# Performance work log

Measured on AMD Instinct MI355X. Metric: run time of the kernel, lower is better.

## Reference

```python
import jax, jax.numpy as jnp
import numpy as np

B, L, D, H = 2, 2048, 512, 8
SAMPLING_FACTOR = 5


def setup_inputs() -> dict:
    key = jax.random.key(0)
    ks = jax.random.split(key, 12)
    L_K = min(8000, L)
    log_L_K = int(np.ceil(np.log1p(L_K)))
    U_part = min(SAMPLING_FACTOR * L * log_L_K, L_K)  # = 2048
    inp = {
        'q': jax.random.normal(ks[0], (B, L, D), jnp.float32),
        'k': jax.random.normal(ks[1], (B, L, D), jnp.float32),
        'v': jax.random.normal(ks[2], (B, L, D), jnp.float32),
        'Wq': jax.random.normal(ks[3], (D, D), jnp.float32) * 0.02,
        'bq': jnp.zeros((D,), jnp.float32),
        'Wk': jax.random.normal(ks[4], (D, D), jnp.float32) * 0.02,
        'bk': jnp.zeros((D,), jnp.float32),
        'Wv': jax.random.normal(ks[5], (D, D), jnp.float32) * 0.02,
        'bv': jnp.zeros((D,), jnp.float32),
        'Wo': jax.random.normal(ks[6], (D, D), jnp.float32) * 0.02,
        'bo': jnp.zeros((D,), jnp.float32),
        'index_sample': jax.random.randint(ks[7], (U_part,), 0, L_K, jnp.int32),
    }
    return inp


def _prob_sparse(qh, Kh, Vh, index_sample):
    # qh, Kh, Vh: [B, H, L, d]
    L_K = min(8000, Kh.shape[2])  # K_sample = K[:, :8000]; L_K = its length
    L_Q = qh.shape[2]
    Ks = Kh[:, :, index_sample, :]                                  # [B,H,U,d]
    QKs = jnp.einsum('bhqd,bhkd->bhqk', qh, Ks)                     # [B,H,Lq,U]
    # M = max - sum/L_K  (source divides by L_K, not U_part)
    M = QKs.max(axis=-1) - QKs.sum(axis=-1) / L_K                   # [B,H,Lq]
    u = min(SAMPLING_FACTOR * int(np.ceil(np.log1p(L_Q))), L_Q)     # = 40
    _, M_top = jax.lax.top_k(-M, u)                                 # topk(largest=False)
    Q_red = jnp.take_along_axis(qh, M_top[..., None], axis=2)       # [B,H,u,d]
    d_k = qh.shape[-1]
    scores = jnp.einsum('bhqd,bhkd->bhqk', Q_red, Kh) / jnp.sqrt(jnp.asarray(d_k, qh.dtype))
    probs = jax.nn.softmax(scores, axis=-1)
    out = jnp.einsum('bhqk,bhkd->bhqd', probs, Vh)                  # [B,H,u,d]
    return out, scores


def reference(q, k, v, Wq, bq, Wk, bk, Wv, bv, Wo, bo, index_sample):
    qp = q @ Wq.T + bq
    kp = k @ Wk.T + bk
    vp = v @ Wv.T + bv
    Bsz, Lq, Dm = qp.shape
    d = Dm // H
    # faithful to source: q is view'd to [B,H,Lq,d] WITHOUT transpose
    qh = qp.reshape(Bsz, H, Lq, d)
    kh = kp.reshape(Bsz, -1, H, d).transpose(0, 2, 1, 3)
    vh = vp.reshape(Bsz, -1, H, d).transpose(0, 2, 1, 3)
    out, _ = _prob_sparse(qh, kh, vh, index_sample)
    u = out.shape[2]
    out = out.transpose(0, 2, 1, 3).reshape(Bsz, u, Dm)             # concat
    return out @ Wo.T + bo                                          # [B,u,D]
```

## Files before the change

### kernel.cpp

```cpp
#include <hip/hip_runtime.h>
#include <math.h>

#define B_ 2
#define L_ 2048
#define D_ 512
#define H_ 8
#define DH 64
#define NS 2048
#define NU 40
#define BHD (L_*D_)
#define QHS (L_*DH)

typedef __attribute__((ext_vector_type(8))) short bf16x8;
typedef __attribute__((ext_vector_type(4))) float f32x4;

__device__ inline float4 ld4(const float* p) { return *reinterpret_cast<const float4*>(p); }

__device__ inline unsigned short hi16(float x) { return (unsigned short)(__float_as_uint(x) >> 16); }
__device__ inline float trunchf(float x) { return __uint_as_float(__float_as_uint(x) & 0xFFFF0000u); }
__device__ inline void tsplit(float x, unsigned short& hs, unsigned short& ms, unsigned short& ls) {
  float h = trunchf(x); hs = hi16(x);
  float r = x - h;
  float m = trunchf(r); ms = hi16(r);
  float r2 = r - m;
  ls = hi16(r2);
}

__global__ __launch_bounds__(256) void proj_mfma(
    const float* __restrict__ qa, const float* __restrict__ ka, const float* __restrict__ va,
    const float* __restrict__ Wq, const float* __restrict__ Wk, const float* __restrict__ Wv,
    const float* __restrict__ bq, const float* __restrict__ bk, const float* __restrict__ bv,
    float* __restrict__ qp, float* __restrict__ kp, float* __restrict__ vp)
{
  __shared__ __align__(16) unsigned short a3[3][128][36];
  __shared__ __align__(16) unsigned short w3[3][128][36];
  const int t = threadIdx.x;
  const int mat = blockIdx.z;
  const float* A    = (mat == 0) ? qa : (mat == 1) ? ka : va;
  const float* W    = (mat == 0) ? Wq : (mat == 1) ? Wk : Wv;
  const float* bias = (mat == 0) ? bq : (mat == 1) ? bk : bv;
  float* C          = (mat == 0) ? qp : (mat == 1) ? kp : vp;
  const int m0 = blockIdx.x * 128, n0 = blockIdx.y * 128;
  const int w = t >> 6, l = t & 63;
  const int wm = w >> 1, wn = w & 1;
  const int lr = l & 15, lg = l >> 4;
  const int srow = t >> 1, sc0 = (t & 1) * 16;

  f32x4 acc[4][4];
#pragma unroll
  for (int i = 0; i < 4; ++i)
#pragma unroll
    for (int j = 0; j < 4; ++j) acc[i][j] = (f32x4){0.f, 0.f, 0.f, 0.f};

  for (int kc = 0; kc < 16; ++kc) {
    const int kb = kc * 32;
    __syncthreads();
    {
      const float* src = A + (size_t)(m0 + srow) * 512 + kb + sc0;
      float xs[16];
#pragma unroll
      for (int i = 0; i < 4; ++i) {
        float4 v4 = ld4(src + 4*i);
        xs[4*i] = v4.x; xs[4*i+1] = v4.y; xs[4*i+2] = v4.z; xs[4*i+3] = v4.w;
      }
#pragma unroll
      for (int hh = 0; hh < 2; ++hh) {
        union { bf16x8 v; unsigned short u[8]; } H, M, L;
#pragma unroll
        for (int e = 0; e < 8; ++e) tsplit(xs[hh*8 + e], H.u[e], M.u[e], L.u[e]);
        *reinterpret_cast<bf16x8*>(&a3[0][srow][sc0 + 8*hh]) = H.v;
        *reinterpret_cast<bf16x8*>(&a3[1][srow][sc0 + 8*hh]) = M.v;
        *reinterpret_cast<bf16x8*>(&a3[2][srow][sc0 + 8*hh]) = L.v;
      }
    }
    {
      const float* src = W + (size_t)(n0 + srow) * 512 + kb + sc0;
      float xs[16];
#pragma unroll
      for (int i = 0; i < 4; ++i) {
        float4 v4 = ld4(src + 4*i);
        xs[4*i] = v4.x; xs[4*i+1] = v4.y; xs[4*i+2] = v4.z; xs[4*i+3] = v4.w;
      }
#pragma unroll
      for (int hh = 0; hh < 2; ++hh) {
        union { bf16x8 v; unsigned short u[8]; } H, M, L;
#pragma unroll
        for (int e = 0; e < 8; ++e) tsplit(xs[hh*8 + e], H.u[e], M.u[e], L.u[e]);
        *reinterpret_cast<bf16x8*>(&w3[0][srow][sc0 + 8*hh]) = H.v;
        *reinterpret_cast<bf16x8*>(&w3[1][srow][sc0 + 8*hh]) = M.v;
        *reinterpret_cast<bf16x8*>(&w3[2][srow][sc0 + 8*hh]) = L.v;
      }
    }
    __syncthreads();

    bf16x8 af[3][4], bf[3][4];
#pragma unroll
    for (int p = 0; p < 3; ++p)
#pragma unroll
      for (int mi = 0; mi < 4; ++mi)
        af[p][mi] = *reinterpret_cast<const bf16x8*>(&a3[p][wm*64 + mi*16 + lr][lg*8]);
#pragma unroll
    for (int p = 0; p < 3; ++p)
#pragma unroll
      for (int ni = 0; ni < 4; ++ni)
        bf[p][ni] = *reinterpret_cast<const bf16x8*>(&w3[p][wn*64 + ni*16 + lr][lg*8]);
#pragma unroll
    for (int mi = 0; mi < 4; ++mi)
#pragma unroll
      for (int ni = 0; ni < 4; ++ni) {
        acc[mi][ni] = __builtin_amdgcn_mfma_f32_16x16x32_bf16(af[0][mi], bf[0][ni], acc[mi][ni], 0, 0, 0);
        acc[mi][ni] = __builtin_amdgcn_mfma_f32_16x16x32_bf16(af[0][mi], bf[1][ni], acc[mi][ni], 0, 0, 0);
        acc[mi][ni] = __builtin_amdgcn_mfma_f32_16x16x32_bf16(af[1][mi], bf[0][ni], acc[mi][ni], 0, 0, 0);
        acc[mi][ni] = __builtin_amdgcn_mfma_f32_16x16x32_bf16(af[1][mi], bf[1][ni], acc[mi][ni], 0, 0, 0);
        acc[mi][ni] = __builtin_amdgcn_mfma_f32_16x16x32_bf16(af[0][mi], bf[2][ni], acc[mi][ni], 0, 0, 0);
        acc[mi][ni] = __builtin_amdgcn_mfma_f32_16x16x32_bf16(af[2][mi], bf[0][ni], acc[mi][ni], 0, 0, 0);
      }
  }
#pragma unroll
  for (int mi = 0; mi < 4; ++mi)
#pragma unroll
    for (int ni = 0; ni < 4; ++ni) {
      const int gn = n0 + wn*64 + ni*16 + lr;
      const float bv_ = bias[gn];
#pragma unroll
      for (int r = 0; r < 4; ++r) {
        const int gm = m0 + wm*64 + mi*16 + lg*4 + r;
        C[(size_t)gm * 512 + gn] = acc[mi][ni][r] + bv_;
      }
    }
}

__global__ __launch_bounds__(1024) void ksum_kernel(const float* __restrict__ kp,
                                                    const int* __restrict__ idx,
                                                    float* __restrict__ ksum) {
  __shared__ float part[16][64];
  const int bh = blockIdx.x;
  const int b = bh >> 3, h = bh & 7;
  const int t = threadIdx.x;
  const int sg = t >> 6, j = t & 63;
  const float* kbase = kp + (size_t)b*BHD + h*DH;
  float a = 0.f;
  for (int s = sg*128; s < sg*128 + 128; ++s)
    a += kbase[(size_t)idx[s]*512 + j];
  part[sg][j] = a;
  __syncthreads();
  if (t < 64) {
    float s = 0.f;
#pragma unroll
    for (int i = 0; i < 16; ++i) s += part[i][t];
    ksum[bh*64 + t] = s;
  }
}

__global__ __launch_bounds__(256) void m_kernel(const float* __restrict__ qp,
                                                const float* __restrict__ kp,
                                                const int* __restrict__ idx,
                                                float* __restrict__ Mp) {
  __shared__ __align__(16) unsigned short k3[3][128][72];
  const int t = threadIdx.x;
  const int bid = blockIdx.x;
  const int bh = bid >> 4, qt = (bid >> 1) & 7, ks = bid & 1;
  const int b = bh >> 3, h = bh & 7;
  const int w = t >> 6, l = t & 63;
  const int lr = l & 15;
  const int lg = l >> 4;

  bf16x8 qf[4][2][3];
  {
    const float* qbase = qp + (size_t)b*BHD + (size_t)h*QHS + (size_t)(qt*256 + w*64 + lr) * 64 + lg*8;
#pragma unroll
    for (int mi = 0; mi < 4; ++mi)
#pragma unroll
      for (int c = 0; c < 2; ++c) {
        const float* src = qbase + mi*16*64 + c*32;
        float4 x0 = ld4(src), x1 = ld4(src + 4);
        float xs[8] = {x0.x, x0.y, x0.z, x0.w, x1.x, x1.y, x1.z, x1.w};
        union { bf16x8 v; unsigned short u[8]; } H, M, L;
#pragma unroll
        for (int e = 0; e < 8; ++e) tsplit(xs[e], H.u[e], M.u[e], L.u[e]);
        qf[mi][c][0] = H.v; qf[mi][c][1] = M.v; qf[mi][c][2] = L.v;
      }
  }

  const float* kbase = kp + (size_t)b*BHD + h*DH;
  const int ib = ks * 1024;
  const int srow = t >> 1, sh = (t & 1) * 32;

  float4 vst[8];
  {
    const int kr = idx[ib + srow];
    const float* src = kbase + (size_t)kr * 512 + sh;
#pragma unroll
    for (int i = 0; i < 8; ++i) vst[i] = ld4(src + 4*i);
  }

  float mx[4][4];
#pragma unroll
  for (int mi = 0; mi < 4; ++mi)
#pragma unroll
    for (int r = 0; r < 4; ++r) mx[mi][r] = -INFINITY;

  for (int tl = 0; tl < 8; ++tl) {
    __syncthreads();
    {
#pragma unroll
      for (int e2 = 0; e2 < 4; ++e2) {
        union { bf16x8 v; unsigned short u[8]; } H, M, L;
        float xs[8] = {vst[2*e2].x, vst[2*e2].y, vst[2*e2].z, vst[2*e2].w,
                       vst[2*e2+1].x, vst[2*e2+1].y, vst[2*e2+1].z, vst[2*e2+1].w};
#pragma unroll
        for (int e = 0; e < 8; ++e) tsplit(xs[e], H.u[e], M.u[e], L.u[e]);
        *reinterpret_cast<bf16x8*>(&k3[0][srow][sh + 8*e2]) = H.v;
        *reinterpret_cast<bf16x8*>(&k3[1][srow][sh + 8*e2]) = M.v;
        *reinterpret_cast<bf16x8*>(&k3[2][srow][sh + 8*e2]) = L.v;
      }
    }
    if (tl < 7) {
      const int kr = idx[ib + (tl+1)*128 + srow];
      const float* src = kbase + (size_t)kr * 512 + sh;
#pragma unroll
      for (int i = 0; i < 8; ++i) vst[i] = ld4(src + 4*i);
    }
    __syncthreads();

    for (int n2 = 0; n2 < 4; ++n2) {
      bf16x8 bf[2][3][2];
#pragma unroll
      for (int ns = 0; ns < 2; ++ns)
#pragma unroll
        for (int p = 0; p < 3; ++p)
#pragma unroll
          for (int c = 0; c < 2; ++c)
            bf[ns][p][c] = *reinterpret_cast<const bf16x8*>(&k3[p][n2*32 + ns*16 + lr][c*32 + lg*8]);
#pragma unroll
      for (int mi = 0; mi < 4; ++mi)
#pragma unroll
        for (int ns = 0; ns < 2; ++ns) {
          f32x4 acc = {0.f, 0.f, 0.f, 0.f};
#pragma unroll
          for (int c = 0; c < 2; ++c) acc = __builtin_amdgcn_mfma_f32_16x16x32_bf16(qf[mi][c][0], bf[ns][0][c], acc, 0, 0, 0);
#pragma unroll
          for (int c = 0; c < 2; ++c) acc = __builtin_amdgcn_mfma_f32_16x16x32_bf16(qf[mi][c][0], bf[ns][1][c], acc, 0, 0, 0);
#pragma unroll
          for (int c = 0; c < 2; ++c) acc = __builtin_amdgcn_mfma_f32_16x16x32_bf16(qf[mi][c][1], bf[ns][0][c], acc, 0, 0, 0);
#pragma unroll
          for (int c = 0; c < 2; ++c) acc = __builtin_amdgcn_mfma_f32_16x16x32_bf16(qf[mi][c][1], bf[ns][1][c], acc, 0, 0, 0);
#pragma unroll
          for (int c = 0; c < 2; ++c) acc = __builtin_amdgcn_mfma_f32_16x16x32_bf16(qf[mi][c][0], bf[ns][2][c], acc, 0, 0, 0);
#pragma unroll
          for (int c = 0; c < 2; ++c) acc = __builtin_amdgcn_mfma_f32_16x16x32_bf16(qf[mi][c][2], bf[ns][0][c], acc, 0, 0, 0);
#pragma unroll
          for (int r = 0; r < 4; ++r) mx[mi][r] = fmaxf(mx[mi][r], acc[r]);
        }
    }
  }

#pragma unroll
  for (int mi = 0; mi < 4; ++mi)
#pragma unroll
    for (int r = 0; r < 4; ++r) {
      float v = mx[mi][r];
      v = fmaxf(v, __shfl_xor(v, 1));
      v = fmaxf(v, __shfl_xor(v, 2));
      v = fmaxf(v, __shfl_xor(v, 4));
      v = fmaxf(v, __shfl_xor(v, 8));
      if (lr == 0)
        Mp[ks*32768 + bh*2048 + qt*256 + w*64 + mi*16 + lg*4 + r] = v;
    }
}

__global__ __launch_bounds__(256) void topk_kernel(const float* __restrict__ qp,
                                                   const float* __restrict__ ksum,
                                                   const float* __restrict__ Mp,
                                                   int* __restrict__ Mtop) {
  __shared__ float ks_s[64];
  __shared__ unsigned hist[256];
  __shared__ int wsum[4];
  __shared__ unsigned bitmap[64];
  __shared__ unsigned long long comb[NU];
  __shared__ int s_sel, s_rem, s_cnt;
  const int bh = blockIdx.x;
  const int b = bh >> 3, h = bh & 7;
  const int t = threadIdx.x;
  if (t < 64) ks_s[t] = ksum[bh*64 + t];
  __syncthreads();

  unsigned mykey[8];
#pragma unroll
  for (int c = 0; c < 8; ++c) {
    const int qi = c * 256 + t;
    const float* qrow = qp + (size_t)b*BHD + (size_t)h*QHS + (size_t)qi * 64;
    float dot = 0.f;
#pragma unroll
    for (int cc = 0; cc < 16; ++cc) {
      float4 q4 = ld4(qrow + 4 * cc);
      dot += q4.x * ks_s[4*cc + 0];
      dot += q4.y * ks_s[4*cc + 1];
      dot += q4.z * ks_s[4*cc + 2];
      dot += q4.w * ks_s[4*cc + 3];
    }
    const float m = fmaxf(Mp[bh*2048 + qi], Mp[32768 + bh*2048 + qi]) - dot * (1.0f/2048.0f);
    const unsigned u = __float_as_uint(m);
    mykey[c] = (u >> 31) ? ~u : (u | 0x80000000u);
  }

  unsigned prefMask = 0u, prefVal = 0u;
  int rem = NU;
  for (int shift = 24; shift >= 0; shift -= 8) {
    hist[t] = 0;
    __syncthreads();
#pragma unroll
    for (int c = 0; c < 8; ++c) {
      const unsigned key = mykey[c];
      if ((key & prefMask) == prefVal)
        atomicAdd(&hist[(key >> shift) & 255], 1u);
    }
    __syncthreads();
    const int binc = (int)hist[t];
    int inc = binc;
#pragma unroll
    for (int off = 1; off < 64; off <<= 1) {
      const int nb = __shfl_up(inc, off);
      if ((t & 63) >= off) inc += nb;
    }
    if ((t & 63) == 63) wsum[t >> 6] = inc;
    __syncthreads();
    int wadd = 0;
    for (int w2 = 0; w2 < (t >> 6); ++w2) wadd += wsum[w2];
    const int incl = inc + wadd;
    const int excl = incl - binc;
    if (excl < rem && rem <= incl) { s_sel = t; s_rem = rem - excl; }
    __syncthreads();
    prefVal |= ((unsigned)s_sel) << shift;
    prefMask |= 0xFFu << shift;
    rem = s_rem;
    __syncthreads();
  }
  const unsigned T = prefVal;

  if (t < 64) bitmap[t] = 0;
  if (t == 0) s_cnt = 0;
  __syncthreads();
#pragma unroll
  for (int c = 0; c < 8; ++c) {
    const unsigned key = mykey[c];
    const int qi = c * 256 + t;
    if (key < T) {
      const int pos = atomicAdd(&s_cnt, 1);
      comb[pos] = ((unsigned long long)key << 11) | (unsigned)qi;
    } else if (key == T) {
      atomicOr(&bitmap[qi >> 5], 1u << (qi & 31));
    }
  }
  __syncthreads();
  if (t == 0) {
    int need = rem, cpos = s_cnt;
    for (int wd = 0; wd < 64 && need > 0; ++wd) {
      unsigned bits = bitmap[wd];
      while (bits && need > 0) {
        const int bit = __ffs(bits) - 1;
        bits &= bits - 1;
        comb[cpos++] = ((unsigned long long)T << 11) | (unsigned)(wd*32 + bit);
        --need;
      }
    }
  }
  __syncthreads();

  if (t < 64) {
    const unsigned long long mine = (t < NU) ? comb[t] : ~0ULL;
    int rank = 0;
#pragma unroll
    for (int step = 1; step < 64; ++step) {
      const unsigned long long other = __shfl(mine, (t + step) & 63);
      rank += (other < mine) ? 1 : 0;
    }
    if (t < NU) Mtop[bh*NU + rank] = (int)(mine & 0x7FFu);
  }
}

__global__ __launch_bounds__(256) void flash_partial(const float* __restrict__ qp,
                                                     const float* __restrict__ kp,
                                                     const float* __restrict__ vp,
                                                     const int* __restrict__ Mtop,
                                                     float* __restrict__ pm,
                                                     float* __restrict__ pl,
                                                     float* __restrict__ pacc) {
  __shared__ float qr[NU][65];
  __shared__ float kv[64][65];
  __shared__ float sl[NU][65];
  __shared__ float ms[NU], ls[NU], fs[NU];
  const int bid = blockIdx.x;
  const int bh = bid >> 4, kt = bid & 15;
  const int b = bh >> 3, h = bh & 7;
  const int t = threadIdx.x;
  const int g = t >> 6, j = t & 63;
  const int r4 = t >> 2, sub = t & 3;

  {
    const float* qbase = qp + (size_t)b*BHD + (size_t)h*QHS;
#pragma unroll
    for (int r = 0; r < 10; ++r) {
      const int q = g*10 + r;
      qr[q][j] = qbase[(size_t)Mtop[bh*NU + q]*64 + j];
    }
  }
  if (t < NU) { ms[t] = -INFINITY; ls[t] = 0.f; }
  float acc[10];
#pragma unroll
  for (int r = 0; r < 10; ++r) acc[r] = 0.f;

  const float* kbase = kp + (size_t)b*BHD + h*DH;
  const float* vbase = vp + (size_t)b*BHD + h*DH;
  const int srow = t >> 2, scb = (t & 3)*16;

  for (int st = 0; st < 2; ++st) {
    const int kb = kt*128 + st*64;
    __syncthreads();
    {
      const float* src = kbase + (size_t)(kb + srow)*512 + scb;
#pragma unroll
      for (int i = 0; i < 4; ++i) {
        float4 v = ld4(src + 4*i);
        kv[srow][scb + 4*i + 0] = v.x;
        kv[srow][scb + 4*i + 1] = v.y;
        kv[srow][scb + 4*i + 2] = v.z;
        kv[srow][scb + 4*i + 3] = v.w;
      }
    }
    __syncthreads();
    {
      float sv[10];
#pragma unroll
      for (int r = 0; r < 10; ++r) {
        const int q = g*10 + r;
        float s = 0.f;
#pragma unroll 8
        for (int jj = 0; jj < 64; ++jj) s += qr[q][jj]*kv[j][jj];
        sv[r] = s * 0.125f;
      }
#pragma unroll
      for (int r = 0; r < 10; ++r) sl[g*10 + r][j] = sv[r];
    }
    __syncthreads();
    float4 vst[4];
    {
      const float* src = vbase + (size_t)(kb + srow)*512 + scb;
#pragma unroll
      for (int i = 0; i < 4; ++i) vst[i] = ld4(src + 4*i);
    }
    if (r4 < NU) {
      float tm = -INFINITY;
#pragma unroll
      for (int c = 0; c < 16; ++c) tm = fmaxf(tm, sl[r4][sub*16 + c]);
      tm = fmaxf(tm, __shfl_xor(tm, 1));
      tm = fmaxf(tm, __shfl_xor(tm, 2));
      const float nm = fmaxf(ms[r4], tm);
      if (sub == 0) { fs[r4] = expf(ms[r4] - nm); ms[r4] = nm; }
    }
    __syncthreads();
    {
#pragma unroll
      for (int r = 0; r < 10; ++r) {
        const int q = g*10 + r;
        acc[r] *= fs[q];
        sl[q][j] = expf(sl[q][j] - ms[q]);
      }
#pragma unroll
      for (int i = 0; i < 4; ++i) {
        kv[srow][scb + 4*i + 0] = vst[i].x;
        kv[srow][scb + 4*i + 1] = vst[i].y;
        kv[srow][scb + 4*i + 2] = vst[i].z;
        kv[srow][scb + 4*i + 3] = vst[i].w;
      }
    }
    __syncthreads();
    if (r4 < NU) {
      float s = 0.f;
#pragma unroll
      for (int c = 0; c < 16; ++c) s += sl[r4][sub*16 + c];
      s += __shfl_xor(s, 1);
      s += __shfl_xor(s, 2);
      if (sub == 0) ls[r4] = ls[r4]*fs[r4] + s;
    }
    {
#pragma unroll 4
      for (int kk = 0; kk < 64; ++kk) {
        const float vv = kv[kk][j];
#pragma unroll
        for (int r = 0; r < 10; ++r) acc[r] += sl[g*10 + r][kk]*vv;
      }
    }
  }
  __syncthreads();
  const size_t base = (size_t)(bh*16 + kt)*NU;
  if (t < NU) { pm[base + t] = ms[t]; pl[base + t] = ls[t]; }
#pragma unroll
  for (int r = 0; r < 10; ++r)
    pacc[(base + g*10 + r)*64 + j] = acc[r];
}

__global__ __launch_bounds__(256) void flash_combine(const float* __restrict__ pm,
                                                     const float* __restrict__ pl,
                                                     const float* __restrict__ pacc,
                                                     float* __restrict__ outc) {
  const int t = threadIdx.x;
  const int qg = t >> 6, j = t & 63;
  const int bh = blockIdx.x / 10;
  const int q  = (blockIdx.x % 10)*4 + qg;
  const int b = bh >> 3, h = bh & 7;
  float m = -INFINITY;
#pragma unroll
  for (int kt = 0; kt < 16; ++kt) m = fmaxf(m, pm[(size_t)(bh*16 + kt)*NU + q]);
  float Lsum = 0.f, num = 0.f;
#pragma unroll
  for (int kt = 0; kt < 16; ++kt) {
    const size_t base = (size_t)(bh*16 + kt)*NU;
    const float w = expf(pm[base + q] - m);
    Lsum += w * pl[base + q];
    num  += w * pacc[(base + q)*64 + j];
  }
  outc[(size_t)(b*NU + q)*512 + h*64 + j] = num / Lsum;
}

__global__ __launch_bounds__(256) void wo_gemm(const float* __restrict__ outc,
                                               const float* __restrict__ Wo,
                                               float* __restrict__ pwo) {
  __shared__ __align__(16) float a_t[80][68];
  __shared__ __align__(16) float w_t[64][68];
  const int t = threadIdx.x;
  const int ty = t >> 4, tx = t & 15;
  const int nt = blockIdx.x, ks = blockIdx.y;
  float acc[5][4];
#pragma unroll
  for (int i = 0; i < 5; ++i)
#pragma unroll
    for (int j = 0; j < 4; ++j) acc[i][j] = 0.f;

  for (int c = 0; c < 2; ++c) {
    const int kb = ks*128 + c*64;
    __syncthreads();
#pragma unroll
    for (int i = 0; i < 20; ++i) {
      const int fi = t + 256*i;
      const int row = fi >> 6, col = fi & 63;
      a_t[row][col] = outc[(size_t)row*512 + kb + col];
    }
#pragma unroll
    for (int i = 0; i < 16; ++i) {
      const int fi = t + 256*i;
      const int row = fi >> 6, col = fi & 63;
      w_t[row][col] = Wo[(size_t)(nt*64 + row)*512 + kb + col];
    }
    __syncthreads();
    for (int gq = 0; gq < 16; ++gq) {
      float4 av[5], wv[4];
#pragma unroll
      for (int i = 0; i < 5; ++i) av[i] = *reinterpret_cast<const float4*>(&a_t[ty + 16*i][4*gq]);
#pragma unroll
      for (int j = 0; j < 4; ++j) wv[j] = *reinterpret_cast<const float4*>(&w_t[tx + 16*j][4*gq]);
#pragma unroll
      for (int i = 0; i < 5; ++i)
#pragma unroll
        for (int j = 0; j < 4; ++j) {
          acc[i][j] += av[i].x * wv[j].x;
          acc[i][j] += av[i].y * wv[j].y;
          acc[i][j] += av[i].z * wv[j].z;
          acc[i][j] += av[i].w * wv[j].w;
        }
    }
  }
#pragma unroll
  for (int i = 0; i < 5; ++i)
#pragma unroll
    for (int j = 0; j < 4; ++j)
      pwo[ks*40960 + (size_t)(ty + 16*i)*512 + nt*64 + tx + 16*j] = acc[i][j];
}

__global__ __launch_bounds__(256) void wo_combine(const float* __restrict__ pwo,
                                                  const float* __restrict__ bo,
                                                  float* __restrict__ out) {
  const int gi = blockIdx.x*256 + threadIdx.x;
  const float4* p = reinterpret_cast<const float4*>(pwo);
  const float4 a = p[gi], b4 = p[10240 + gi], c4 = p[20480 + gi], d4 = p[30720 + gi];
  const float4 bb = ld4(bo + 4*(gi & 127));
  float4 o;
  o.x = a.x + b4.x + c4.x + d4.x + bb.x;
  o.y = a.y + b4.y + c4.y + d4.y + bb.y;
  o.z = a.z + b4.z + c4.z + d4.z + bb.z;
  o.w = a.w + b4.w + c4.w + d4.w + bb.w;
  reinterpret_cast<float4*>(out)[gi] = o;
}

extern "C" void kernel_launch(void* const* d_in, const int* in_sizes, int n_in,
                              void* d_out, int out_size, void* d_ws, size_t ws_size,
                              hipStream_t stream) {
  const float* q  = (const float*)d_in[0];
  const float* k  = (const float*)d_in[1];
  const float* v  = (const float*)d_in[2];
  const float* Wq = (const float*)d_in[3];
  const float* bq = (const float*)d_in[4];
  const float* Wk = (const float*)d_in[5];
  const float* bk = (const float*)d_in[6];
  const float* Wv = (const float*)d_in[7];
  const float* bv = (const float*)d_in[8];
  const float* Wo = (const float*)d_in[9];
  const float* bo = (const float*)d_in[10];
  const int*  idx = (const int*)d_in[11];

  float* ws   = (float*)d_ws;
  float* qp   = ws;
  float* kp   = ws + 2097152;
  float* vp   = ws + 4194304;
  float* ksum = ws + 6291456;
  int*   Mtop = (int*)(ws + 6292480);
  float* pm   = ws + 6293120;
  float* pl   = ws + 6303360;
  float* pacc = ws + 6313600;
  float* outc = ws + 6968960;
  float* Mp   = pm;
  float* pwo  = pm;

  const dim3 blk(256);
  proj_mfma<<<dim3(32, 4, 3), blk, 0, stream>>>(q, k, v, Wq, Wk, Wv, bq, bk, bv, qp, kp, vp);
  ksum_kernel<<<dim3(16), dim3(1024), 0, stream>>>(kp, idx, ksum);
  m_kernel<<<dim3(256), blk, 0, stream>>>(qp, kp, idx, Mp);
  topk_kernel<<<dim3(16), blk, 0, stream>>>(qp, ksum, Mp, Mtop);
  flash_partial<<<dim3(256), blk, 0, stream>>>(qp, kp, vp, Mtop, pm, pl, pacc);
  flash_combine<<<dim3(160), blk, 0, stream>>>(pm, pl, pacc, outc);
  wo_gemm<<<dim3(8, 4), blk, 0, stream>>>(outc, Wo, pwo);
  wo_combine<<<dim3(40), blk, 0, stream>>>(pwo, bo, (float*)d_out);
}
```

Measured before the change: 199.1 us.

## Pre-split weights into bf16 triplets in MFMA fragment layout before projection

Adds a wsplit kernel that converts Wq/Wk/Wv once into hi/mid/lo bf16 pieces, stored directly in the per-lane MFMA B-fragment order. The projection GEMM then loads these fragments straight from global memory into registers, instead of having every M-tile block re-split the weights and stage them through shared memory. This removes redundant split work and half the LDS traffic. In exchange it adds a kernel launch, extra global reads of 16-bit data per block, and a fallback path of three launch pairs when the workspace is small.

```diff
diff --git a/kernel.cpp b/kernel.cpp
--- a/kernel.cpp
+++ b/kernel.cpp
@@ -10,6 +10,7 @@
 #define NU 40
 #define BHD (L_*D_)
 #define QHS (L_*DH)
+#define WSPM 786432
 
 typedef __attribute__((ext_vector_type(8))) short bf16x8;
 typedef __attribute__((ext_vector_type(4))) float f32x4;
@@ -26,21 +27,57 @@
   ls = hi16(r2);
 }
 
-__global__ __launch_bounds__(256) void proj_mfma(
+__global__ __launch_bounds__(256) void wsplit(const float* __restrict__ Wq,
+                                              const float* __restrict__ Wk,
+                                              const float* __restrict__ Wv,
+                                              unsigned short* __restrict__ dst,
+                                              int matArg) {
+  const int mat = (matArg >= 0) ? matArg : (int)blockIdx.y;
+  const float* W = (mat == 0) ? Wq : (mat == 1) ? Wk : Wv;
+  unsigned short* d = dst + ((matArg >= 0) ? 0 : (size_t)mat * WSPM);
+  const int t = threadIdx.x;
+  const int nt = blockIdx.x >> 3, g16 = blockIdx.x & 7;
+  const int kc = t >> 4, lr = t & 15;
+  const int n = nt*128 + g16*16 + lr;
+  const float* src = W + (size_t)n*512 + kc*32;
+  float xs[32];
+#pragma unroll
+  for (int i = 0; i < 8; ++i) {
+    float4 v4 = ld4(src + 4*i);
+    xs[4*i] = v4.x; xs[4*i+1] = v4.y; xs[4*i+2] = v4.z; xs[4*i+3] = v4.w;
+  }
+  unsigned short Hs[32], Ms[32], Ls[32];
+#pragma unroll
+  for (int e = 0; e < 32; ++e) tsplit(xs[e], Hs[e], Ms[e], Ls[e]);
+#pragma unroll
+  for (int p = 0; p < 3; ++p) {
+    const unsigned short* sp = (p == 0) ? Hs : (p == 1) ? Ms : Ls;
+    unsigned short* base = d + ((size_t)((p*4 + nt)*8 + g16)*16 + kc)*512;
+#pragma unroll
+    for (int lg = 0; lg < 4; ++lg) {
+      union { bf16x8 v; unsigned short u[8]; } P;
+#pragma unroll
+      for (int e = 0; e < 8; ++e) P.u[e] = sp[lg*8 + e];
+      *reinterpret_cast<bf16x8*>(base + (lr + 16*lg)*8) = P.v;
+    }
+  }
+}
+
+__global__ __launch_bounds__(256) void proj_mfma2(
     const float* __restrict__ qa, const float* __restrict__ ka, const float* __restrict__ va,
-    const float* __restrict__ Wq, const float* __restrict__ Wk, const float* __restrict__ Wv,
+    const unsigned short* __restrict__ wsp,
     const float* __restrict__ bq, const float* __restrict__ bk, const float* __restrict__ bv,
-    float* __restrict__ qp, float* __restrict__ kp, float* __restrict__ vp)
+    float* __restrict__ qp, float* __restrict__ kp, float* __restrict__ vp,
+    int matArg)
 {
   __shared__ __align__(16) unsigned short a3[3][128][36];
-  __shared__ __align__(16) unsigned short w3[3][128][36];
-  const int t = threadIdx.x;
-  const int mat = blockIdx.z;
+  const int t = threadIdx.x;
+  const int mat = (matArg >= 0) ? matArg : (int)blockIdx.z;
   const float* A    = (mat == 0) ? qa : (mat == 1) ? ka : va;
-  const float* W    = (mat == 0) ? Wq : (mat == 1) ? Wk : Wv;
   const float* bias = (mat == 0) ? bq : (mat == 1) ? bk : bv;
   float* C          = (mat == 0) ? qp : (mat == 1) ? kp : vp;
-  const int m0 = blockIdx.x * 128, n0 = blockIdx.y * 128;
+  const unsigned short* wspm = wsp + ((matArg >= 0) ? 0 : (size_t)mat * WSPM);
+  const int m0 = blockIdx.x * 128, nt = blockIdx.y;
   const int w = t >> 6, l = t & 63;
   const int wm = w >> 1, wn = w & 1;
   const int lr = l & 15, lg = l >> 4;
@@ -53,10 +90,16 @@
     for (int j = 0; j < 4; ++j) acc[i][j] = (f32x4){0.f, 0.f, 0.f, 0.f};
 
   for (int kc = 0; kc < 16; ++kc) {
-    const int kb = kc * 32;
-    __syncthreads();
+    __syncthreads();
+    bf16x8 bw[3][4];
+#pragma unroll
+    for (int p = 0; p < 3; ++p)
+#pragma unroll
+      for (int ni = 0; ni < 4; ++ni)
+        bw[p][ni] = *reinterpret_cast<const bf16x8*>(
+            wspm + ((size_t)((p*4 + nt)*8 + wn*4 + ni)*16 + kc)*512 + l*8);
     {
-      const float* src = A + (size_t)(m0 + srow) * 512 + kb + sc0;
+      const float* src = A + (size_t)(m0 + srow) * 512 + kc*32 + sc0;
       float xs[16];
 #pragma unroll
       for (int i = 0; i < 4; ++i) {
@@ -73,54 +116,29 @@
         *reinterpret_cast<bf16x8*>(&a3[2][srow][sc0 + 8*hh]) = L.v;
       }
     }
-    {
-      const float* src = W + (size_t)(n0 + srow) * 512 + kb + sc0;
-      float xs[16];
-#pragma unroll
-      for (int i = 0; i < 4; ++i) {
-        float4 v4 = ld4(src + 4*i);
-        xs[4*i] = v4.x; xs[4*i+1] = v4.y; xs[4*i+2] = v4.z; xs[4*i+3] = v4.w;
-      }
-#pragma unroll
-      for (int hh = 0; hh < 2; ++hh) {
-        union { bf16x8 v; unsigned short u[8]; } H, M, L;
-#pragma unroll
-        for (int e = 0; e < 8; ++e) tsplit(xs[hh*8 + e], H.u[e], M.u[e], L.u[e]);
-        *reinterpret_cast<bf16x8*>(&w3[0][srow][sc0 + 8*hh]) = H.v;
-        *reinterpret_cast<bf16x8*>(&w3[1][srow][sc0 + 8*hh]) = M.v;
-        *reinterpret_cast<bf16x8*>(&w3[2][srow][sc0 + 8*hh]) = L.v;
-      }
-    }
-    __syncthreads();
-
-    bf16x8 af[3][4], bf[3][4];
-#pragma unroll
-    for (int p = 0; p < 3; ++p)
-#pragma unroll
-      for (int mi = 0; mi < 4; ++mi)
-        af[p][mi] = *reinterpret_cast<const bf16x8*>(&a3[p][wm*64 + mi*16 + lr][lg*8]);
-#pragma unroll
-    for (int p = 0; p < 3; ++p)
-#pragma unroll
-      for (int ni = 0; ni < 4; ++ni)
-        bf[p][ni] = *reinterpret_cast<const bf16x8*>(&w3[p][wn*64 + ni*16 + lr][lg*8]);
-#pragma unroll
-    for (int mi = 0; mi < 4; ++mi)
+    __syncthreads();
+
+#pragma unroll
+    for (int mi = 0; mi < 4; ++mi) {
+      bf16x8 a0 = *reinterpret_cast<const bf16x8*>(&a3[0][wm*64 + mi*16 + lr][lg*8]);
+      bf16x8 a1 = *reinterpret_cast<const bf16x8*>(&a3[1][wm*64 + mi*16 + lr][lg*8]);
+      bf16x8 a2 = *reinterpret_cast<const bf16x8*>(&a3[2][wm*64 + mi*16 + lr][lg*8]);
 #pragma unroll
       for (int ni = 0; ni < 4; ++ni) {
-        acc[mi][ni] = __builtin_amdgcn_mfma_f32_16x16x32_bf16(af[0][mi], bf[0][ni], acc[mi][ni], 0, 0, 0);
-        acc[mi][ni] = __builtin_amdgcn_mfma_f32_16x16x32_bf16(af[0][mi], bf[1][ni], acc[mi][ni], 0, 0, 0);
-        acc[mi][ni] = __builtin_amdgcn_mfma_f32_16x16x32_bf16(af[1][mi], bf[0][ni], acc[mi][ni], 0, 0, 0);
-        acc[mi][ni] = __builtin_amdgcn_mfma_f32_16x16x32_bf16(af[1][mi], bf[1][ni], acc[mi][ni], 0, 0, 0);
-        acc[mi][ni] = __builtin_amdgcn_mfma_f32_16x16x32_bf16(af[0][mi], bf[2][ni], acc[mi][ni], 0, 0, 0);
-        acc[mi][ni] = __builtin_amdgcn_mfma_f32_16x16x32_bf16(af[2][mi], bf[0][ni], acc[mi][ni], 0, 0, 0);
-      }
+        acc[mi][ni] = __builtin_amdgcn_mfma_f32_16x16x32_bf16(a0, bw[0][ni], acc[mi][ni], 0, 0, 0);
+        acc[mi][ni] = __builtin_amdgcn_mfma_f32_16x16x32_bf16(a0, bw[1][ni], acc[mi][ni], 0, 0, 0);
+        acc[mi][ni] = __builtin_amdgcn_mfma_f32_16x16x32_bf16(a1, bw[0][ni], acc[mi][ni], 0, 0, 0);
+        acc[mi][ni] = __builtin_amdgcn_mfma_f32_16x16x32_bf16(a1, bw[1][ni], acc[mi][ni], 0, 0, 0);
+        acc[mi][ni] = __builtin_amdgcn_mfma_f32_16x16x32_bf16(a0, bw[2][ni], acc[mi][ni], 0, 0, 0);
+        acc[mi][ni] = __builtin_amdgcn_mfma_f32_16x16x32_bf16(a2, bw[0][ni], acc[mi][ni], 0, 0, 0);
+      }
+    }
   }
 #pragma unroll
   for (int mi = 0; mi < 4; ++mi)
 #pragma unroll
     for (int ni = 0; ni < 4; ++ni) {
-      const int gn = n0 + wn*64 + ni*16 + lr;
+      const int gn = nt*128 + wn*64 + ni*16 + lr;
       const float bv_ = bias[gn];
 #pragma unroll
       for (int r = 0; r < 4; ++r) {
@@ -620,9 +638,19 @@
   float* outc = ws + 6968960;
   float* Mp   = pm;
   float* pwo  = pm;
+  unsigned short* wsp = (unsigned short*)(ws + 6291456);
 
   const dim3 blk(256);
-  proj_mfma<<<dim3(32, 4, 3), blk, 0, stream>>>(q, k, v, Wq, Wk, Wv, bq, bk, bv, qp, kp, vp);
+  const bool bigws = (ws_size >= (size_t)7471104 * 4);
+  if (bigws) {
+    wsplit<<<dim3(32, 3), blk, 0, stream>>>(Wq, Wk, Wv, wsp, -1);
+    proj_mfma2<<<dim3(32, 4, 3), blk, 0, stream>>>(q, k, v, wsp, bq, bk, bv, qp, kp, vp, -1);
+  } else {
+    for (int m = 0; m < 3; ++m) {
+      wsplit<<<dim3(32, 1), blk, 0, stream>>>(Wq, Wk, Wv, wsp, m);
+      proj_mfma2<<<dim3(32, 4, 1), blk, 0, stream>>>(q, k, v, wsp, bq, bk, bv, qp, kp, vp, m);
+    }
+  }
   ksum_kernel<<<dim3(16), dim3(1024), 0, stream>>>(kp, idx, ksum);
   m_kernel<<<dim3(256), blk, 0, stream>>>(qp, kp, idx, Mp);
   topk_kernel<<<dim3(16), blk, 0, stream>>>(qp, ksum, Mp, Mtop);
```

After: 196.2 us. About the same (-1.5%).
